# Performance work log

Measured on AMD Instinct MI355X. Metric: run time of the kernel, lower is better.

The kernel has to match this reference:

```python
import jax, jax.numpy as jnp
import numpy as np

N = 100000
E = 640000
IN_CH = 256
OUT_CH = 64
HID = 2 * OUT_CH  # 128


def setup_inputs() -> dict:
    key = jax.random.key(0)
    ks = jax.random.split(key, 8)
    x = jax.random.normal(ks[0], (N, IN_CH), dtype=jnp.float32)
    edge_index = jax.random.randint(ks[1], (2, E), 0, N, dtype=jnp.int32)
    s = 1.0 / np.sqrt(IN_CH)
    W1 = jax.random.uniform(ks[2], (IN_CH, HID), jnp.float32, -s, s)
    b1 = jnp.zeros((HID,), jnp.float32)
    s2 = 1.0 / np.sqrt(HID)
    W_mu = jax.random.uniform(ks[3], (HID, OUT_CH), jnp.float32, -s2, s2)
    b_mu = jnp.zeros((OUT_CH,), jnp.float32)
    W_ls = jax.random.uniform(ks[4], (HID, OUT_CH), jnp.float32, -s2, s2)
    b_ls = jnp.zeros((OUT_CH,), jnp.float32)
    return {"x": x, "W1": W1, "b1": b1, "W_mu": W_mu, "b_mu": b_mu,
            "W_ls": W_ls, "b_ls": b_ls, "edge_index": edge_index}


def _gcn_norm(edge_index, n_nodes):
    # PyG GCNConv default: add self-loops, symmetric normalization D^-1/2 A D^-1/2
    loops = jnp.arange(n_nodes, dtype=edge_index.dtype)
    src = jnp.concatenate([edge_index[0], loops])
    dst = jnp.concatenate([edge_index[1], loops])
    deg = jax.ops.segment_sum(jnp.ones_like(dst, jnp.float32), dst, num_segments=n_nodes)
    dinv = jnp.where(deg > 0, jax.lax.rsqrt(deg), 0.0)
    norm = dinv[src] * dinv[dst]  # [E+N]
    return src, dst, norm


def _gcn_conv(x, W, b, src, dst, norm, n_nodes):
    h = x @ W                                   # [N, F_out]
    msg = h[src] * norm[:, None]                # [E+N, F_out] gather
    out = jax.ops.segment_sum(msg, dst, num_segments=n_nodes)  # scatter-add
    return out + b


def reference(x, W1, b1, W_mu, b_mu, W_ls, b_ls, edge_index):
    src, dst, norm = _gcn_norm(edge_index, N)
    h = jax.nn.relu(_gcn_conv(x, W1, b1, src, dst, norm, N))
    mu = _gcn_conv(h, W_mu, b_mu, src, dst, norm, N)
    logstd = _gcn_conv(h, W_ls, b_ls, src, dst, norm, N)
    return mu, logstd
```

## Files before the change

### kernel.cpp

```cpp
#include <hip/hip_runtime.h>
#include <math.h>

#define NN 100000
#define EE 640000
#define INCH 256
#define HIDC 128
#define OUTC 64
#define NCHUNK ((NN + 255) / 256)

typedef __attribute__((ext_vector_type(8))) short short8;
typedef __attribute__((ext_vector_type(8))) unsigned short ushort8;
typedef __attribute__((ext_vector_type(4))) float floatx4;

__device__ __forceinline__ short f2bf(float f) {
    unsigned u = __float_as_uint(f);
    u += 0x7fff + ((u >> 16) & 1);
    return (short)(u >> 16);
}

__device__ __forceinline__ float bf2f(unsigned short u) {
    return __uint_as_float(((unsigned)u) << 16);
}

__global__ void k_deg_zero(int* __restrict__ deg) {
    int i = blockIdx.x * 256 + threadIdx.x;
    if (i < NN) deg[i] = 0;
}

__global__ void k_deg_count(const int* __restrict__ dstp, int* __restrict__ deg) {
    int e = blockIdx.x * 256 + threadIdx.x;
    if (e < EE) atomicAdd(&deg[dstp[e]], 1);
}

__global__ __launch_bounds__(256) void k_scan1(const int* __restrict__ deg,
                                               int* __restrict__ partials) {
    int i = blockIdx.x * 256 + threadIdx.x;
    int v = (i < NN) ? deg[i] : 0;
    for (int o = 32; o; o >>= 1) v += __shfl_down(v, o, 64);
    __shared__ int sm[4];
    if ((threadIdx.x & 63) == 0) sm[threadIdx.x >> 6] = v;
    __syncthreads();
    if (threadIdx.x == 0) partials[blockIdx.x] = sm[0] + sm[1] + sm[2] + sm[3];
}

__global__ __launch_bounds__(512) void k_scan2(int* __restrict__ partials) {
    __shared__ int sm[512];
    int t = threadIdx.x;
    int v = (t < NCHUNK) ? partials[t] : 0;
    sm[t] = v;
    __syncthreads();
    for (int o = 1; o < 512; o <<= 1) {
        int add = (t >= o) ? sm[t - o] : 0;
        __syncthreads();
        sm[t] += add;
        __syncthreads();
    }
    if (t < NCHUNK) partials[t] = sm[t] - v;
}

__global__ __launch_bounds__(256) void k_scan3(const int* __restrict__ deg,
                                               const int* __restrict__ partials,
                                               int* __restrict__ row_off,
                                               int* __restrict__ cursor,
                                               float* __restrict__ dinv) {
    int t = threadIdx.x;
    int i = blockIdx.x * 256 + t;
    int v = (i < NN) ? deg[i] : 0;
    __shared__ int sm[256];
    sm[t] = v;
    __syncthreads();
    for (int o = 1; o < 256; o <<= 1) {
        int add = (t >= o) ? sm[t - o] : 0;
        __syncthreads();
        sm[t] += add;
        __syncthreads();
    }
    if (i < NN) {
        int excl = partials[blockIdx.x] + sm[t] - v;
        row_off[i] = excl;
        cursor[i] = excl;
        dinv[i] = rsqrtf((float)(v + 1));
    }
}

__global__ void k_fill(const int* __restrict__ srcp, const int* __restrict__ dstp,
                       int* __restrict__ cursor, int* __restrict__ esrc) {
    int e = blockIdx.x * 256 + threadIdx.x;
    if (e < EE) {
        int d = dstp[e];
        int pos = atomicAdd(&cursor[d], 1);
        esrc[pos] = srcp[e];
    }
}

__global__ void k_prep(const float* __restrict__ W1,
                       const float* __restrict__ Wmu, const float* __restrict__ bmu,
                       const float* __restrict__ Wls, const float* __restrict__ bls,
                       short* __restrict__ wt, short* __restrict__ wct,
                       float* __restrict__ bcat) {
    int i = blockIdx.x * 256 + threadIdx.x;
    if (i < 32768) {
        int n = i >> 8, k = i & 255;
        wt[i] = f2bf(W1[k * HIDC + n]);
    } else if (i < 32768 + 16384) {
        int j = i - 32768;
        int n = j >> 7, k = j & 127;
        float v = (n < OUTC) ? Wmu[k * OUTC + n] : Wls[k * OUTC + (n - OUTC)];
        wct[j] = f2bf(v);
    } else if (i < 32768 + 16384 + 128) {
        int c = i - (32768 + 16384);
        bcat[c] = (c < OUTC) ? bmu[c] : bls[c - OUTC];
    }
}

__global__ __launch_bounds__(256) void k_mgemm1(const float* __restrict__ x,
                                                const short* __restrict__ wt,
                                                short* __restrict__ out) {
    int wave = threadIdx.x >> 6;
    int lane = threadIdx.x & 63;
    int m = lane & 15, quad = lane >> 4;
    int rbase = blockIdx.x * 128 + wave * 32;
    int r0c = min(rbase + m, NN - 1);
    int r1c = min(rbase + 16 + m, NN - 1);
    const float* xr0 = x + (size_t)r0c * INCH + quad * 8;
    const float* xr1 = x + (size_t)r1c * INCH + quad * 8;
    floatx4 acc0[8], acc1[8];
#pragma unroll
    for (int i = 0; i < 8; i++) { acc0[i] = (floatx4)(0.f); acc1[i] = (floatx4)(0.f); }
#pragma unroll
    for (int k0 = 0; k0 < INCH; k0 += 32) {
        float4 p00 = *(const float4*)(xr0 + k0);
        float4 p01 = *(const float4*)(xr0 + k0 + 4);
        float4 p10 = *(const float4*)(xr1 + k0);
        float4 p11 = *(const float4*)(xr1 + k0 + 4);
        short8 a0, a1;
        a0[0] = f2bf(p00.x); a0[1] = f2bf(p00.y); a0[2] = f2bf(p00.z); a0[3] = f2bf(p00.w);
        a0[4] = f2bf(p01.x); a0[5] = f2bf(p01.y); a0[6] = f2bf(p01.z); a0[7] = f2bf(p01.w);
        a1[0] = f2bf(p10.x); a1[1] = f2bf(p10.y); a1[2] = f2bf(p10.z); a1[3] = f2bf(p10.w);
        a1[4] = f2bf(p11.x); a1[5] = f2bf(p11.y); a1[6] = f2bf(p11.z); a1[7] = f2bf(p11.w);
        const short* wq = wt + k0 + quad * 8 + (size_t)m * INCH;
#pragma unroll
        for (int nt = 0; nt < 8; nt++) {
            short8 b = *(const short8*)(wq + (size_t)nt * 16 * INCH);
            acc0[nt] = __builtin_amdgcn_mfma_f32_16x16x32_bf16(a0, b, acc0[nt], 0, 0, 0);
            acc1[nt] = __builtin_amdgcn_mfma_f32_16x16x32_bf16(a1, b, acc1[nt], 0, 0, 0);
        }
    }
    int rs0 = rbase + quad * 4;
    int rs1 = rbase + 16 + quad * 4;
#pragma unroll
    for (int nt = 0; nt < 8; nt++) {
        int c = nt * 16 + m;
#pragma unroll
        for (int r = 0; r < 4; r++) {
            int rr = rs0 + r;
            if (rr < NN) out[(size_t)rr * HIDC + c] = f2bf(acc0[nt][r]);
            int rr2 = rs1 + r;
            if (rr2 < NN) out[(size_t)rr2 * HIDC + c] = f2bf(acc1[nt][r]);
        }
    }
}

__global__ __launch_bounds__(256) void k_mgemm2(const short* __restrict__ agg,
                                                const short* __restrict__ wct,
                                                const float* __restrict__ bcat,
                                                float* __restrict__ out) {
    int wave = threadIdx.x >> 6;
    int lane = threadIdx.x & 63;
    int m = lane & 15, quad = lane >> 4;
    int rbase = blockIdx.x * 128 + wave * 32;
    int r0c = min(rbase + m, NN - 1);
    int r1c = min(rbase + 16 + m, NN - 1);
    const short* ar0 = agg + (size_t)r0c * HIDC + quad * 8;
    const short* ar1 = agg + (size_t)r1c * HIDC + quad * 8;
    floatx4 acc0[8], acc1[8];
#pragma unroll
    for (int i = 0; i < 8; i++) { acc0[i] = (floatx4)(0.f); acc1[i] = (floatx4)(0.f); }
#pragma unroll
    for (int k0 = 0; k0 < HIDC; k0 += 32) {
        short8 a0 = *(const short8*)(ar0 + k0);
        short8 a1 = *(const short8*)(ar1 + k0);
        const short* wq = wct + k0 + quad * 8 + (size_t)m * HIDC;
#pragma unroll
        for (int nt = 0; nt < 8; nt++) {
            short8 b = *(const short8*)(wq + (size_t)nt * 16 * HIDC);
            acc0[nt] = __builtin_amdgcn_mfma_f32_16x16x32_bf16(a0, b, acc0[nt], 0, 0, 0);
            acc1[nt] = __builtin_amdgcn_mfma_f32_16x16x32_bf16(a1, b, acc1[nt], 0, 0, 0);
        }
    }
    int rs0 = rbase + quad * 4;
    int rs1 = rbase + 16 + quad * 4;
#pragma unroll
    for (int nt = 0; nt < 8; nt++) {
        int c = nt * 16 + m;
        float bv = bcat[c];
        float* obase = (c < OUTC) ? (out + c) : (out + (size_t)NN * OUTC + (c - OUTC));
#pragma unroll
        for (int r = 0; r < 4; r++) {
            int rr = rs0 + r;
            if (rr < NN) obase[(size_t)rr * OUTC] = acc0[nt][r] + bv;
            int rr2 = rs1 + r;
            if (rr2 < NN) obase[(size_t)rr2 * OUTC] = acc1[nt][r] + bv;
        }
    }
}

template <bool RELU>
__global__ __launch_bounds__(256) void k_gather(const short* __restrict__ feat,
                                                const int* __restrict__ esrc,
                                                const int* __restrict__ row_off,
                                                const int* __restrict__ deg,
                                                const float* __restrict__ dinv,
                                                const float* __restrict__ bias,
                                                short* __restrict__ out) {
    int gid = blockIdx.x * 256 + threadIdx.x;
    int d = gid >> 4;
    int l = threadIdx.x & 15;
    if (d >= NN) return;
    const ushort8* fp = (const ushort8*)feat;
    float dd = dinv[d];
    float sw = dd * dd;
    ushort8 sv = fp[(size_t)d * 16 + l];
    float acc[8];
#pragma unroll
    for (int i = 0; i < 8; i++) acc[i] = bf2f(sv[i]) * sw;
    int off = row_off[d];
    int cnt = deg[d];
    for (int base = 0; base < cnt; base += 16) {
        int mm = min(16, cnt - base);
        int sj = (l < mm) ? esrc[off + base + l] : 0;
        float dj = (l < mm) ? dinv[sj] : 0.f;
        for (int j = 0; j < mm; j++) {
            int s = __shfl(sj, j, 16);
            float nw = __shfl(dj, j, 16) * dd;
            ushort8 v = fp[(size_t)s * 16 + l];
#pragma unroll
            for (int i = 0; i < 8; i++) acc[i] = fmaf(bf2f(v[i]), nw, acc[i]);
        }
    }
    if (RELU) {
        float4 b0 = *(const float4*)(bias + l * 8);
        float4 b1 = *(const float4*)(bias + l * 8 + 4);
        acc[0] = fmaxf(acc[0] + b0.x, 0.f);
        acc[1] = fmaxf(acc[1] + b0.y, 0.f);
        acc[2] = fmaxf(acc[2] + b0.z, 0.f);
        acc[3] = fmaxf(acc[3] + b0.w, 0.f);
        acc[4] = fmaxf(acc[4] + b1.x, 0.f);
        acc[5] = fmaxf(acc[5] + b1.y, 0.f);
        acc[6] = fmaxf(acc[6] + b1.z, 0.f);
        acc[7] = fmaxf(acc[7] + b1.w, 0.f);
    }
    ushort8 o;
#pragma unroll
    for (int i = 0; i < 8; i++) o[i] = (unsigned short)f2bf(acc[i]);
    ((ushort8*)out)[(size_t)d * 16 + l] = o;
}

extern "C" void kernel_launch(void* const* d_in, const int* in_sizes, int n_in,
                              void* d_out, int out_size, void* d_ws, size_t ws_size,
                              hipStream_t stream) {
    const float* x   = (const float*)d_in[0];
    const float* W1  = (const float*)d_in[1];
    const float* b1  = (const float*)d_in[2];
    const float* Wmu = (const float*)d_in[3];
    const float* bmu = (const float*)d_in[4];
    const float* Wls = (const float*)d_in[5];
    const float* bls = (const float*)d_in[6];
    const int*   ei  = (const int*)d_in[7];
    const int* srcp = ei;
    const int* dstp = ei + EE;

    float* out = (float*)d_out;

    char* wsb = (char*)d_ws;
    short* bufA    = (short*)wsb;
    short* bufH    = bufA + (size_t)NN * HIDC;
    int*   deg     = (int*)(bufH + (size_t)NN * HIDC);
    int*   row_off = deg + NN;
    int*   cursor  = row_off + NN;
    float* dinv    = (float*)(cursor + NN);
    int*   esrc    = (int*)(dinv + NN);
    int*   partials = esrc + EE;
    short* wt      = (short*)(partials + NCHUNK + 1);
    short* wct     = wt + 128 * 256;
    float* bcat    = (float*)(wct + 128 * 128);

    const int nb_n = (NN + 255) / 256;
    const int nb_e = (EE + 255) / 256;
    const int nb_g = (NN * 16) / 256;
    const int nb_m = (NN + 127) / 128;

    k_deg_zero<<<nb_n, 256, 0, stream>>>(deg);
    k_deg_count<<<nb_e, 256, 0, stream>>>(dstp, deg);
    k_scan1<<<NCHUNK, 256, 0, stream>>>(deg, partials);
    k_scan2<<<1, 512, 0, stream>>>(partials);
    k_scan3<<<NCHUNK, 256, 0, stream>>>(deg, partials, row_off, cursor, dinv);
    k_fill<<<nb_e, 256, 0, stream>>>(srcp, dstp, cursor, esrc);
    k_prep<<<193, 256, 0, stream>>>(W1, Wmu, bmu, Wls, bls, wt, wct, bcat);

    k_mgemm1<<<nb_m, 256, 0, stream>>>(x, wt, bufA);
    k_gather<true><<<nb_g, 256, 0, stream>>>(bufA, esrc, row_off, deg, dinv, b1, bufH);

    k_gather<false><<<nb_g, 256, 0, stream>>>(bufH, esrc, row_off, deg, dinv, nullptr, bufA);
    k_mgemm2<<<nb_m, 256, 0, stream>>>(bufA, wct, bcat, out);
}
```

Measured before the change: 383.2 us.

## Split GEMM column tiles across waves and unroll gather neighbor loads by four

The GEMM kernels now assign each block 64 rows, with the four waves splitting the output columns into two halves instead of each wave covering all 128 columns. This halves the accumulator registers per wave and doubles the block count for better occupancy, though each wave's row data is now loaded twice per block. Separately, the neighbor-aggregation loop is unrolled by four, with remainders of two and one, so several independent feature-row gathers are in flight before their FMAs. This aims to hide memory latency in the gather step.

Measured after the change: 379.0 us. About the same (-1.1%).

```diff
diff --git a/kernel.cpp b/kernel.cpp
--- a/kernel.cpp
+++ b/kernel.cpp
@@ -118,15 +118,17 @@
                                                 short* __restrict__ out) {
     int wave = threadIdx.x >> 6;
     int lane = threadIdx.x & 63;
+    int rhalf = wave & 1, chalf = wave >> 1;
     int m = lane & 15, quad = lane >> 4;
-    int rbase = blockIdx.x * 128 + wave * 32;
+    int rbase = blockIdx.x * 64 + rhalf * 32;
     int r0c = min(rbase + m, NN - 1);
     int r1c = min(rbase + 16 + m, NN - 1);
     const float* xr0 = x + (size_t)r0c * INCH + quad * 8;
     const float* xr1 = x + (size_t)r1c * INCH + quad * 8;
-    floatx4 acc0[8], acc1[8];
-#pragma unroll
-    for (int i = 0; i < 8; i++) { acc0[i] = (floatx4)(0.f); acc1[i] = (floatx4)(0.f); }
+    const short* wbase = wt + quad * 8 + (size_t)m * INCH + (size_t)(chalf * 4) * 16 * INCH;
+    floatx4 acc0[4], acc1[4];
+#pragma unroll
+    for (int i = 0; i < 4; i++) { acc0[i] = (floatx4)(0.f); acc1[i] = (floatx4)(0.f); }
 #pragma unroll
     for (int k0 = 0; k0 < INCH; k0 += 32) {
         float4 p00 = *(const float4*)(xr0 + k0);
@@ -138,9 +140,9 @@
         a0[4] = f2bf(p01.x); a0[5] = f2bf(p01.y); a0[6] = f2bf(p01.z); a0[7] = f2bf(p01.w);
         a1[0] = f2bf(p10.x); a1[1] = f2bf(p10.y); a1[2] = f2bf(p10.z); a1[3] = f2bf(p10.w);
         a1[4] = f2bf(p11.x); a1[5] = f2bf(p11.y); a1[6] = f2bf(p11.z); a1[7] = f2bf(p11.w);
-        const short* wq = wt + k0 + quad * 8 + (size_t)m * INCH;
-#pragma unroll
-        for (int nt = 0; nt < 8; nt++) {
+        const short* wq = wbase + k0;
+#pragma unroll
+        for (int nt = 0; nt < 4; nt++) {
             short8 b = *(const short8*)(wq + (size_t)nt * 16 * INCH);
             acc0[nt] = __builtin_amdgcn_mfma_f32_16x16x32_bf16(a0, b, acc0[nt], 0, 0, 0);
             acc1[nt] = __builtin_amdgcn_mfma_f32_16x16x32_bf16(a1, b, acc1[nt], 0, 0, 0);
@@ -149,8 +151,8 @@
     int rs0 = rbase + quad * 4;
     int rs1 = rbase + 16 + quad * 4;
 #pragma unroll
-    for (int nt = 0; nt < 8; nt++) {
-        int c = nt * 16 + m;
+    for (int nt = 0; nt < 4; nt++) {
+        int c = (chalf * 4 + nt) * 16 + m;
 #pragma unroll
         for (int r = 0; r < 4; r++) {
             int rr = rs0 + r;
@@ -167,22 +169,24 @@
                                                 float* __restrict__ out) {
     int wave = threadIdx.x >> 6;
     int lane = threadIdx.x & 63;
+    int rhalf = wave & 1, chalf = wave >> 1;
     int m = lane & 15, quad = lane >> 4;
-    int rbase = blockIdx.x * 128 + wave * 32;
+    int rbase = blockIdx.x * 64 + rhalf * 32;
     int r0c = min(rbase + m, NN - 1);
     int r1c = min(rbase + 16 + m, NN - 1);
     const short* ar0 = agg + (size_t)r0c * HIDC + quad * 8;
     const short* ar1 = agg + (size_t)r1c * HIDC + quad * 8;
-    floatx4 acc0[8], acc1[8];
-#pragma unroll
-    for (int i = 0; i < 8; i++) { acc0[i] = (floatx4)(0.f); acc1[i] = (floatx4)(0.f); }
+    const short* wbase = wct + quad * 8 + (size_t)m * HIDC + (size_t)(chalf * 4) * 16 * HIDC;
+    floatx4 acc0[4], acc1[4];
+#pragma unroll
+    for (int i = 0; i < 4; i++) { acc0[i] = (floatx4)(0.f); acc1[i] = (floatx4)(0.f); }
 #pragma unroll
     for (int k0 = 0; k0 < HIDC; k0 += 32) {
         short8 a0 = *(const short8*)(ar0 + k0);
         short8 a1 = *(const short8*)(ar1 + k0);
-        const short* wq = wct + k0 + quad * 8 + (size_t)m * HIDC;
-#pragma unroll
-        for (int nt = 0; nt < 8; nt++) {
+        const short* wq = wbase + k0;
+#pragma unroll
+        for (int nt = 0; nt < 4; nt++) {
             short8 b = *(const short8*)(wq + (size_t)nt * 16 * HIDC);
             acc0[nt] = __builtin_amdgcn_mfma_f32_16x16x32_bf16(a0, b, acc0[nt], 0, 0, 0);
             acc1[nt] = __builtin_amdgcn_mfma_f32_16x16x32_bf16(a1, b, acc1[nt], 0, 0, 0);
@@ -191,8 +195,8 @@
     int rs0 = rbase + quad * 4;
     int rs1 = rbase + 16 + quad * 4;
 #pragma unroll
-    for (int nt = 0; nt < 8; nt++) {
-        int c = nt * 16 + m;
+    for (int nt = 0; nt < 4; nt++) {
+        int c = (chalf * 4 + nt) * 16 + m;
         float bv = bcat[c];
         float* obase = (c < OUTC) ? (out + c) : (out + (size_t)NN * OUTC + (c - OUTC));
 #pragma unroll
@@ -230,12 +234,48 @@
         int mm = min(16, cnt - base);
         int sj = (l < mm) ? esrc[off + base + l] : 0;
         float dj = (l < mm) ? dinv[sj] : 0.f;
-        for (int j = 0; j < mm; j++) {
-            int s = __shfl(sj, j, 16);
-            float nw = __shfl(dj, j, 16) * dd;
-            ushort8 v = fp[(size_t)s * 16 + l];
-#pragma unroll
-            for (int i = 0; i < 8; i++) acc[i] = fmaf(bf2f(v[i]), nw, acc[i]);
+        int j = 0;
+        for (; j + 4 <= mm; j += 4) {
+            int s0 = __shfl(sj, j + 0, 16);
+            int s1 = __shfl(sj, j + 1, 16);
+            int s2 = __shfl(sj, j + 2, 16);
+            int s3 = __shfl(sj, j + 3, 16);
+            float n0 = __shfl(dj, j + 0, 16) * dd;
+            float n1 = __shfl(dj, j + 1, 16) * dd;
+            float n2 = __shfl(dj, j + 2, 16) * dd;
+            float n3 = __shfl(dj, j + 3, 16) * dd;
+            ushort8 v0 = fp[(size_t)s0 * 16 + l];
+            ushort8 v1 = fp[(size_t)s1 * 16 + l];
+            ushort8 v2 = fp[(size_t)s2 * 16 + l];
+            ushort8 v3 = fp[(size_t)s3 * 16 + l];
+#pragma unroll
+            for (int i = 0; i < 8; i++) acc[i] = fmaf(bf2f(v0[i]), n0, acc[i]);
+#pragma unroll
+            for (int i = 0; i < 8; i++) acc[i] = fmaf(bf2f(v1[i]), n1, acc[i]);
+#pragma unroll
+            for (int i = 0; i < 8; i++) acc[i] = fmaf(bf2f(v2[i]), n2, acc[i]);
+#pragma unroll
+            for (int i = 0; i < 8; i++) acc[i] = fmaf(bf2f(v3[i]), n3, acc[i]);
+        }
+        if (j + 2 <= mm) {
+            int s0 = __shfl(sj, j + 0, 16);
+            int s1 = __shfl(sj, j + 1, 16);
+            float n0 = __shfl(dj, j + 0, 16) * dd;
+            float n1 = __shfl(dj, j + 1, 16) * dd;
+            ushort8 v0 = fp[(size_t)s0 * 16 + l];
+            ushort8 v1 = fp[(size_t)s1 * 16 + l];
+#pragma unroll
+            for (int i = 0; i < 8; i++) acc[i] = fmaf(bf2f(v0[i]), n0, acc[i]);
+#pragma unroll
+            for (int i = 0; i < 8; i++) acc[i] = fmaf(bf2f(v1[i]), n1, acc[i]);
+            j += 2;
+        }
+        if (j < mm) {
+            int s0 = __shfl(sj, j, 16);
+            float n0 = __shfl(dj, j, 16) * dd;
+            ushort8 v0 = fp[(size_t)s0 * 16 + l];
+#pragma unroll
+            for (int i = 0; i < 8; i++) acc[i] = fmaf(bf2f(v0[i]), n0, acc[i]);
         }
     }
     if (RELU) {
@@ -288,7 +328,7 @@
     const int nb_n = (NN + 255) / 256;
     const int nb_e = (EE + 255) / 256;
     const int nb_g = (NN * 16) / 256;
-    const int nb_m = (NN + 127) / 128;
+    const int nb_m = (NN + 63) / 64;
 
     k_deg_zero<<<nb_n, 256, 0, stream>>>(deg);
     k_deg_count<<<nb_e, 256, 0, stream>>>(dstp, deg);
```
